# Optimization experiments

Measured on AMD Instinct MI355X. Metric: run time of the kernel, lower is better.

Reference implementation:

```python
import jax, jax.numpy as jnp
import numpy as np

N = 20000   # nodes
E = 40000   # directed edges
F_IN = 13   # dataset.num_features
G = 1000    # graphs in batch
DIMS = [(13, 32), (32, 64), (64, 64)]  # (M_in, M_out) per NNConv layer


def setup_inputs() -> dict:
    key = jax.random.key(0)
    ks = list(jax.random.split(key, 32))
    inp = {}
    inp["x"] = jax.random.normal(ks[0], (N, F_IN), jnp.float32)
    inp["edge_index"] = jax.random.randint(ks[1], (2, E), 0, N, dtype=jnp.int32)
    inp["edge_attr"] = jax.random.uniform(ks[2], (E, 5), dtype=jnp.float32)
    inp["batch"] = jnp.sort(jax.random.randint(ks[3], (N,), 0, G, dtype=jnp.int32))
    i = 4
    for l, (mi, mo) in enumerate(DIMS):
        inp[f"w1_{l}"] = jax.random.normal(ks[i], (5, 128), jnp.float32) / np.sqrt(5.0).astype(np.float32); i += 1
        inp[f"b1_{l}"] = jnp.zeros((128,), jnp.float32)
        inp[f"w2_{l}"] = jax.random.normal(ks[i], (128, mi * mo), jnp.float32) / np.sqrt(128.0).astype(np.float32); i += 1
        inp[f"b2_{l}"] = jnp.zeros((mi * mo,), jnp.float32)
        inp[f"root_{l}"] = jax.random.normal(ks[i], (mi, mo), jnp.float32) / np.sqrt(float(mi)).astype(np.float32); i += 1
        inp[f"bias_{l}"] = jnp.zeros((mo,), jnp.float32)
    inp["fc1_w"] = jax.random.normal(ks[i], (64, 32), jnp.float32) / 8.0; i += 1
    inp["fc1_b"] = jnp.zeros((32,), jnp.float32)
    inp["fc2_w"] = jax.random.normal(ks[i], (32, 16), jnp.float32) / np.sqrt(32.0).astype(np.float32); i += 1
    inp["fc2_b"] = jnp.zeros((16,), jnp.float32)
    inp["fc3_w"] = jax.random.normal(ks[i], (16, 1), jnp.float32) / 4.0; i += 1
    inp["fc3_b"] = jnp.zeros((1,), jnp.float32)
    return inp


def _nnconv(x, src, dst, edge_attr, w1, b1, w2, b2, root, bias, mi, mo):
    # edge MLP: [E,5] -> [E,128] -> [E, mi*mo] per-edge weight matrices
    h = jax.nn.relu(edge_attr @ w1 + b1)
    We = (h @ w2 + b2).reshape(-1, mi, mo)          # [E, mi, mo]
    msg = jnp.einsum('ei,eio->eo', x[src], We)      # gather + per-edge matmul
    agg = jax.ops.segment_sum(msg, dst, num_segments=x.shape[0])  # scatter-add
    return x @ root + agg + bias                    # NNConv root weight + bias


def _forward(x, edge_index, edge_attr, batch, convs, fc1_w, fc1_b, fc2_w, fc2_b, fc3_w, fc3_b):
    src, dst = edge_index[0], edge_index[1]
    for (mi, mo), (w1, b1, w2, b2, root, bias) in zip(DIMS, convs):
        x = jax.nn.elu(_nnconv(x, src, dst, edge_attr, w1, b1, w2, b2, root, bias, mi, mo))
    # scatter_mean pooling over graphs
    sums = jax.ops.segment_sum(x, batch, num_segments=G)
    cnt = jax.ops.segment_sum(jnp.ones((x.shape[0],), x.dtype), batch, num_segments=G)
    xg = sums / jnp.maximum(cnt, 1.0)[:, None]
    xg = jax.nn.elu(xg @ fc1_w + fc1_b)
    xg = jax.nn.elu(xg @ fc2_w + fc2_b)
    return (xg @ fc3_w + fc3_b).reshape(-1)


def reference(x, edge_index, edge_attr, batch,
              w1_0, b1_0, w2_0, b2_0, root_0, bias_0,
              w1_1, b1_1, w2_1, b2_1, root_1, bias_1,
              w1_2, b1_2, w2_2, b2_2, root_2, bias_2,
              fc1_w, fc1_b, fc2_w, fc2_b, fc3_w, fc3_b):
    convs = [(w1_0, b1_0, w2_0, b2_0, root_0, bias_0),
             (w1_1, b1_1, w2_1, b2_1, root_1, bias_1),
             (w1_2, b1_2, w2_2, b2_2, root_2, bias_2)]
    return _forward(x, edge_index, edge_attr, batch, convs,
                    fc1_w, fc1_b, fc2_w, fc2_b, fc3_w, fc3_b)
```

## Files before the change

### kernel.cpp

```cpp
#include <hip/hip_runtime.h>
#include <stdint.h>
#include <math.h>

typedef _Float16 half8_t __attribute__((ext_vector_type(8)));
typedef float floatx4 __attribute__((ext_vector_type(4)));

#define NN 20000
#define NE 40000
#define NG 1000
#define NBLK 313
#define NSPLIT 4

__global__ __launch_bounds__(256) void prep_fused_kernel(
    const float* __restrict__ x, _Float16* __restrict__ e16,
    const float* __restrict__ w2a, const float* __restrict__ b2a, _Float16* __restrict__ oa,
    const float* __restrict__ w2b, const float* __restrict__ b2b, _Float16* __restrict__ ob,
    const float* __restrict__ w2c, const float* __restrict__ b2c, _Float16* __restrict__ oc,
    int* __restrict__ deg)
{
  if (blockIdx.x < 1250) {
    int idx = blockIdx.x * 256 + threadIdx.x;
    int n = idx >> 4, i = idx & 15;
    e16[idx] = (i < 13) ? (_Float16)x[(size_t)n * 13 + i] : (_Float16)0.f;
    return;
  }
  if (blockIdx.x >= 1680) {
    int n = (blockIdx.x - 1680) * 256 + threadIdx.x;
    if (n < NN) deg[n] = 0;
    return;
  }
  const int TOT0 = 68 * 2 * 64, TOT1 = 132 * 4 * 64, TOT2 = 264 * 4 * 64;
  int idx = (blockIdx.x - 1250) * 256 + threadIdx.x;
  const float *w2, *b2; _Float16* op; int mi, mo, mpsh, CT;
  if (idx < TOT0) { w2 = w2a; b2 = b2a; op = oa; mi = 13; mo = 32; mpsh = 4; CT = 2; }
  else if (idx < TOT0 + TOT1) { idx -= TOT0; w2 = w2b; b2 = b2b; op = ob; mi = 32; mo = 64; mpsh = 5; CT = 4; }
  else if (idx < TOT0 + TOT1 + TOT2) { idx -= TOT0 + TOT1; w2 = w2c; b2 = b2c; op = oc; mi = 64; mo = 64; mpsh = 6; CT = 4; }
  else return;
  int l = idx & 63;
  int ct = (idx >> 6) % CT;
  int c = idx / (64 * CT);
  int q = l >> 4;
  int n = ct * 16 + (l & 15);
  int mask = (1 << mpsh) - 1;
  half8_t v;
#pragma unroll
  for (int j = 0; j < 8; ++j) {
    int r = c * 32 + q * 8 + j;
    int k = r >> mpsh, i = r & mask;
    float f = 0.f;
    if (i < mi) {
      if (k < 128) f = w2[(size_t)(k * mi + i) * mo + n];
      else if (k == 128) f = b2[(size_t)i * mo + n];
    }
    v[j] = (_Float16)f;
  }
  *(half8_t*)(op + (size_t)idx * 8) = v;
}

__global__ __launch_bounds__(256) void deg_kernel(const int* __restrict__ dst, int* __restrict__ deg) {
  int e = blockIdx.x * 256 + threadIdx.x;
  if (e < NE) atomicAdd(&deg[dst[e]], 1);
}

__global__ __launch_bounds__(1024) void scan_kernel(
    const int* __restrict__ deg, int* __restrict__ row_ptr, int* __restrict__ cursor)
{
  constexpr int CH = 20;
  __shared__ int wsum[16];
  int t = threadIdx.x;
  int lane = t & 63, w = t >> 6;
  int base = t * CH;
  int local[CH];
#pragma unroll
  for (int i = 0; i < CH; ++i) {
    int n = base + i;
    local[i] = (n < NN) ? deg[n] : 0;
  }
  int s = 0;
#pragma unroll
  for (int i = 0; i < CH; ++i) s += local[i];
  int sc = s;
#pragma unroll
  for (int d = 1; d < 64; d <<= 1) {
    int v = __shfl_up(sc, d, 64);
    if (lane >= d) sc += v;
  }
  if (lane == 63) wsum[w] = sc;
  __syncthreads();
  if (w == 0 && lane < 16) {
    int v = wsum[lane];
    int scc = v;
#pragma unroll
    for (int d = 1; d < 16; d <<= 1) {
      int u = __shfl_up(scc, d, 64);
      if (lane >= d) scc += u;
    }
    wsum[lane] = scc - v;
  }
  __syncthreads();
  int run = wsum[w] + (sc - s);
#pragma unroll
  for (int i = 0; i < CH; ++i) {
    int n = base + i;
    if (n < NN) { row_ptr[n] = run; cursor[n] = run; run += local[i]; }
    else if (n == NN) row_ptr[NN] = run;
  }
}

__global__ __launch_bounds__(256) void fill_kernel(
    const int* __restrict__ dst, int* __restrict__ cursor, int* __restrict__ eids)
{
  int e = blockIdx.x * 256 + threadIdx.x;
  if (e < NE) { int p = atomicAdd(&cursor[dst[e]], 1); eids[p] = e; }
}

template <int MIP, int MO, int NCC, int KCNT>
__global__ __launch_bounds__(256, 4) void msg9_kernel(
    const float* __restrict__ ea, const float* __restrict__ w1,
    const float* __restrict__ b1, const _Float16* __restrict__ xe,
    const int* __restrict__ src,
    const _Float16* __restrict__ w2h, _Float16* __restrict__ msgp)
{
  constexpr int EPB = 128;
  constexpr int CT = MO / 16;
  constexpr int CHB = CT * 1024;
  constexpr int XV = (MIP == 64) ? 2 : 1;
  constexpr int KH = (KCNT + 1) >> 1;

  __shared__ uint4 wsb[2][CHB / 16];
  __shared__ _Float16 h16[KCNT * EPB];
  __shared__ float w1s[5 * 128 + 128];

  const int t = threadIdx.x;
  const int wave = t >> 6, lane = t & 63;
  const int l15 = lane & 15, q = lane >> 4;
  const int split = blockIdx.x / NBLK;
  const int e0 = (blockIdx.x % NBLK) * EPB;
  const int c0 = NCC * split;
  const int kg0 = KCNT * split;

  const char* wgp = (const char*)w2h + (size_t)c0 * CHB;
  uint4 ra4, rb4; uint2 ra2, rb2;
  if constexpr (CT == 4) {
    ra4 = *(const uint4*)(wgp + t * 16);
    rb4 = *(const uint4*)(wgp + CHB + t * 16);
  } else {
    ra2 = *(const uint2*)(wgp + t * 8);
    rb2 = *(const uint2*)(wgp + CHB + t * 8);
  }

  const int wbase = wave * 32;
  half8_t xf[2][XV];
#pragma unroll
  for (int s = 0; s < 2; ++s) {
    int eg = e0 + wbase + s * 16 + l15; if (eg >= NE) eg = NE - 1;
    const _Float16* xr = xe + (size_t)src[eg] * MIP;
    int i0 = (MIP == 16) ? (q & 1) * 8 : q * 8;
    xf[s][0] = *(const half8_t*)(xr + i0);
    if constexpr (MIP == 64)
      xf[s][XV - 1] = *(const half8_t*)(xr + 32 + q * 8);
  }

  const int te = t & 127;
  float ear[5];
  {
    int eg = e0 + te; if (eg >= NE) eg = NE - 1;
#pragma unroll
    for (int j = 0; j < 5; ++j) ear[j] = ea[(size_t)eg * 5 + j];
  }
  for (int i = t; i < 768; i += 256) w1s[i] = (i < 640) ? w1[i] : b1[i - 640];
  __syncthreads();

  {
    int kh = t >> 7;
    int klo = kh * KH;
    int khi = klo + KH; if (khi > KCNT) khi = KCNT;
    for (int kl = klo; kl < khi; ++kl) {
      int kg = kg0 + kl;
      float v;
      if (kg < 128) {
        v = w1s[640 + kg];
#pragma unroll
        for (int j = 0; j < 5; ++j) v = fmaf(ear[j], w1s[j * 128 + kg], v);
        v = fmaxf(v, 0.f);
      } else v = (kg == 128) ? 1.f : 0.f;
      h16[kl * EPB + te] = (_Float16)v;
    }
  }
  __syncthreads();

  floatx4 acc[2][CT];
#pragma unroll
  for (int s = 0; s < 2; ++s)
#pragma unroll
    for (int b = 0; b < CT; ++b) acc[s][b] = (floatx4){0.f, 0.f, 0.f, 0.f};

#pragma unroll 2
  for (int cc = 0; cc < NCC; ++cc) {
    const bool odd = (cc & 1) != 0;
    if constexpr (CT == 4) wsb[cc & 1][t] = odd ? rb4 : ra4;
    else ((uint2*)wsb[cc & 1])[t] = odd ? rb2 : ra2;
    if (cc + 2 < NCC) {
      const char* np = wgp + (size_t)(cc + 2) * CHB;
      if constexpr (CT == 4) {
        if (odd) rb4 = *(const uint4*)(np + t * 16); else ra4 = *(const uint4*)(np + t * 16);
      } else {
        if (odd) rb2 = *(const uint2*)(np + t * 8); else ra2 = *(const uint2*)(np + t * 8);
      }
    }
    __syncthreads();
    const _Float16* wb = (const _Float16*)wsb[cc & 1];
    half8_t bf[CT];
#pragma unroll
    for (int b = 0; b < CT; ++b)
      bf[b] = *(const half8_t*)(wb + (b * 64 + lane) * 8);
    int kl;
    if constexpr (MIP == 64) kl = cc >> 1;
    else if constexpr (MIP == 32) kl = cc;
    else kl = 2 * cc + (q >> 1);
#pragma unroll
    for (int s = 0; s < 2; ++s) {
      _Float16 hv = h16[kl * EPB + wbase + s * 16 + l15];
      half8_t af;
      if constexpr (MIP == 64) af = xf[s][cc & 1] * hv;
      else af = xf[s][0] * hv;
#pragma unroll
      for (int b = 0; b < CT; ++b)
        acc[s][b] = __builtin_amdgcn_mfma_f32_16x16x32_f16(af, bf[b], acc[s][b], 0, 0, 0);
    }
  }

#pragma unroll
  for (int s = 0; s < 2; ++s) {
    int rowb = wbase + s * 16 + q * 4;
#pragma unroll
    for (int b = 0; b < CT; ++b) {
      int n = b * 16 + l15;
#pragma unroll
      for (int r = 0; r < 4; ++r) {
        int row = rowb + r;
        int e = e0 + row;
        if (e < NE) msgp[((size_t)e * NSPLIT + split) * MO + n] = (_Float16)acc[s][b][r];
      }
    }
  }
}

template <int MIP, int NCC, int KCNT>
__global__ __launch_bounds__(256, 4) void msg9p_kernel(
    const float* __restrict__ ea, const float* __restrict__ w1,
    const float* __restrict__ b1, const _Float16* __restrict__ xe,
    const int* __restrict__ src,
    const _Float16* __restrict__ w2h, _Float16* __restrict__ msgp)
{
  constexpr int EPB = 128;
  constexpr int MO = 64;
  constexpr int CT = 4;
  constexpr int CHB = 4096;
  constexpr int XV = (MIP == 64) ? 2 : 1;
  constexpr int KH = (KCNT + 1) >> 1;
  static_assert((NCC & 1) == 0, "NCC must be even for paired chunks");

  __shared__ uint4 wsb[2][2][CHB / 16];
  __shared__ _Float16 h16[KCNT * EPB];
  __shared__ float w1s[5 * 128 + 128];

  const int t = threadIdx.x;
  const int wave = t >> 6, lane = t & 63;
  const int l15 = lane & 15, q = lane >> 4;
  const int split = blockIdx.x / NBLK;
  const int e0 = (blockIdx.x % NBLK) * EPB;
  const int c0 = NCC * split;
  const int kg0 = KCNT * split;

  const char* wgp = (const char*)w2h + (size_t)c0 * CHB;
  uint4 pA0 = *(const uint4*)(wgp + 0 * CHB + t * 16);
  uint4 pA1 = *(const uint4*)(wgp + 1 * CHB + t * 16);
  uint4 pB0 = *(const uint4*)(wgp + 2 * CHB + t * 16);
  uint4 pB1 = *(const uint4*)(wgp + 3 * CHB + t * 16);

  const int wbase = wave * 32;
  half8_t xf[2][XV];
#pragma unroll
  for (int s = 0; s < 2; ++s) {
    int eg = e0 + wbase + s * 16 + l15; if (eg >= NE) eg = NE - 1;
    const _Float16* xr = xe + (size_t)src[eg] * MIP;
    xf[s][0] = *(const half8_t*)(xr + q * 8);
    if constexpr (MIP == 64)
      xf[s][XV - 1] = *(const half8_t*)(xr + 32 + q * 8);
  }

  const int te = t & 127;
  float ear[5];
  {
    int eg = e0 + te; if (eg >= NE) eg = NE - 1;
#pragma unroll
    for (int j = 0; j < 5; ++j) ear[j] = ea[(size_t)eg * 5 + j];
  }
  for (int i = t; i < 768; i += 256) w1s[i] = (i < 640) ? w1[i] : b1[i - 640];
  __syncthreads();

  {
    int kh = t >> 7;
    int klo = kh * KH;
    int khi = klo + KH; if (khi > KCNT) khi = KCNT;
    for (int kl = klo; kl < khi; ++kl) {
      int kg = kg0 + kl;
      float v;
      if (kg < 128) {
        v = w1s[640 + kg];
#pragma unroll
        for (int j = 0; j < 5; ++j) v = fmaf(ear[j], w1s[j * 128 + kg], v);
        v = fmaxf(v, 0.f);
      } else v = (kg == 128) ? 1.f : 0.f;
      h16[kl * EPB + te] = (_Float16)v;
    }
  }
  __syncthreads();

  floatx4 acc[2][CT];
#pragma unroll
  for (int s = 0; s < 2; ++s)
#pragma unroll
    for (int b = 0; b < CT; ++b) acc[s][b] = (floatx4){0.f, 0.f, 0.f, 0.f};

#pragma unroll 2
  for (int ci = 0; ci < NCC / 2; ++ci) {
    const bool odd = (ci & 1) != 0;
    wsb[ci & 1][0][t] = odd ? pB0 : pA0;
    wsb[ci & 1][1][t] = odd ? pB1 : pA1;
    if (2 * ci + 4 < NCC) {
      const char* np = wgp + (size_t)(2 * ci + 4) * CHB;
      if (odd) pB0 = *(const uint4*)(np + t * 16); else pA0 = *(const uint4*)(np + t * 16);
    }
    if (2 * ci + 5 < NCC) {
      const char* np = wgp + (size_t)(2 * ci + 5) * CHB;
      if (odd) pB1 = *(const uint4*)(np + t * 16); else pA1 = *(const uint4*)(np + t * 16);
    }
    __syncthreads();
#pragma unroll
    for (int u = 0; u < 2; ++u) {
      const int cc = 2 * ci + u;
      const _Float16* wbu = (const _Float16*)wsb[ci & 1][u];
      half8_t bf[CT];
#pragma unroll
      for (int b = 0; b < CT; ++b)
        bf[b] = *(const half8_t*)(wbu + (b * 64 + lane) * 8);
      int kl;
      if constexpr (MIP == 64) kl = cc >> 1;
      else kl = cc;
#pragma unroll
      for (int s = 0; s < 2; ++s) {
        _Float16 hv = h16[kl * EPB + wbase + s * 16 + l15];
        half8_t af;
        if constexpr (MIP == 64) af = xf[s][cc & 1] * hv;
        else af = xf[s][0] * hv;
#pragma unroll
        for (int b = 0; b < CT; ++b)
          acc[s][b] = __builtin_amdgcn_mfma_f32_16x16x32_f16(af, bf[b], acc[s][b], 0, 0, 0);
      }
    }
  }

#pragma unroll
  for (int s = 0; s < 2; ++s) {
    int rowb = wbase + s * 16 + q * 4;
#pragma unroll
    for (int b = 0; b < CT; ++b) {
      int n = b * 16 + l15;
#pragma unroll
      for (int r = 0; r < 4; ++r) {
        int row = rowb + r;
        int e = e0 + row;
        if (e < NE) msgp[((size_t)e * NSPLIT + split) * MO + n] = (_Float16)acc[s][b][r];
      }
    }
  }
}

template <int MIN_, int XST, int MO, int FINAL>
__global__ __launch_bounds__(256) void gather_kernel(
    const _Float16* __restrict__ e16in, const float* __restrict__ root,
    const float* __restrict__ bias, const int* __restrict__ row_ptr,
    const int* __restrict__ eids, const _Float16* __restrict__ msgp,
    _Float16* __restrict__ oute, float* __restrict__ outf)
{
  constexpr int NPB = 256 / MO;
  int n = blockIdx.x * NPB + threadIdx.x / MO;
  int o = threadIdx.x % MO;
  if (n >= NN) return;
  float a = bias[o];
#pragma unroll
  for (int i = 0; i < MIN_; ++i)
    a = fmaf((float)e16in[(size_t)n * XST + i], root[i * MO + o], a);
  int r0 = row_ptr[n], r1 = row_ptr[n + 1];
  for (int j = r0; j < r1; ++j) {
    int e = eids[j];
    const _Float16* ep = msgp + (size_t)e * NSPLIT * MO + o;
#pragma unroll
    for (int s = 0; s < NSPLIT; ++s)
      a += (float)ep[s * MO];
  }
  if constexpr (FINAL) {
    outf[(size_t)n * MO + o] = a;
  } else {
    float v = a > 0.f ? a : (expf(a) - 1.f);
    oute[(size_t)n * MO + o] = (_Float16)v;
  }
}

__global__ __launch_bounds__(64) void pool_fc_kernel(
    const float* __restrict__ xn2, const int* __restrict__ batch,
    const float* __restrict__ f1w, const float* __restrict__ f1b,
    const float* __restrict__ f2w, const float* __restrict__ f2b,
    const float* __restrict__ f3w, const float* __restrict__ f3b,
    float* __restrict__ out)
{
  __shared__ float xg[64]; __shared__ float a1[32]; __shared__ float a2[16];
  int g = blockIdx.x, t = threadIdx.x;
  int lo = 0, hi = NN;
  while (lo < hi) { int m = (lo + hi) >> 1; if (batch[m] < g) lo = m + 1; else hi = m; }
  int start = lo; hi = NN;
  while (lo < hi) { int m = (lo + hi) >> 1; if (batch[m] <= g) lo = m + 1; else hi = m; }
  int end = lo;
  float acc = 0.f;
  for (int n = start; n < end; ++n) {
    float v = xn2[(size_t)n * 64 + t];
    acc += v > 0.f ? v : (expf(v) - 1.f);
  }
  float c = (end > start) ? (float)(end - start) : 1.f;
  xg[t] = acc / c;
  __syncthreads();
  if (t < 32) {
    float a = f1b[t];
    for (int i = 0; i < 64; ++i) a = fmaf(xg[i], f1w[i * 32 + t], a);
    a1[t] = a > 0.f ? a : (expf(a) - 1.f);
  }
  __syncthreads();
  if (t < 16) {
    float a = f2b[t];
    for (int i = 0; i < 32; ++i) a = fmaf(a1[i], f2w[i * 16 + t], a);
    a2[t] = a > 0.f ? a : (expf(a) - 1.f);
  }
  __syncthreads();
  if (t == 0) {
    float a = f3b[0];
    for (int i = 0; i < 16; ++i) a = fmaf(a2[i], f3w[i], a);
    out[g] = a;
  }
}

extern "C" void kernel_launch(void* const* d_in, const int* in_sizes, int n_in,
                              void* d_out, int out_size, void* d_ws, size_t ws_size,
                              hipStream_t stream)
{
  const float* x_in  = (const float*)d_in[0];
  const int*   ei    = (const int*)d_in[1];
  const float* ea    = (const float*)d_in[2];
  const int*   batch = (const int*)d_in[3];
  const float* W1[3] = {(const float*)d_in[4],  (const float*)d_in[10], (const float*)d_in[16]};
  const float* B1[3] = {(const float*)d_in[5],  (const float*)d_in[11], (const float*)d_in[17]};
  const float* W2[3] = {(const float*)d_in[6],  (const float*)d_in[12], (const float*)d_in[18]};
  const float* B2[3] = {(const float*)d_in[7],  (const float*)d_in[13], (const float*)d_in[19]};
  const float* RT[3] = {(const float*)d_in[8],  (const float*)d_in[14], (const float*)d_in[20]};
  const float* BS[3] = {(const float*)d_in[9],  (const float*)d_in[15], (const float*)d_in[21]};
  const float* f1w = (const float*)d_in[22]; const float* f1b = (const float*)d_in[23];
  const float* f2w = (const float*)d_in[24]; const float* f2b = (const float*)d_in[25];
  const float* f3w = (const float*)d_in[26]; const float* f3b = (const float*)d_in[27];

  char* ws = (char*)d_ws;
  size_t off = 0;
  auto alloc = [&](size_t bytes) { void* p = ws + off; off += (bytes + 255) & ~(size_t)255; return p; };
  float*    xn2   = (float*)alloc((size_t)NN * 64 * 4);
  _Float16* e16_0 = (_Float16*)alloc((size_t)NN * 16 * 2);
  _Float16* e16_1 = (_Float16*)alloc((size_t)NN * 32 * 2);
  _Float16* e16_2 = (_Float16*)alloc((size_t)NN * 64 * 2);
  _Float16* w2h0  = (_Float16*)alloc((size_t)68 * 2048);
  _Float16* w2h1  = (_Float16*)alloc((size_t)132 * 4096);
  _Float16* w2h2  = (_Float16*)alloc((size_t)264 * 4096);
  _Float16* msgp  = (_Float16*)alloc((size_t)NSPLIT * NE * 64 * 2);
  int*      deg     = (int*)alloc((size_t)NN * 4);
  int*      row_ptr = (int*)alloc((size_t)(NN + 1) * 4);
  int*      cursor  = (int*)alloc((size_t)NN * 4);
  int*      eids    = (int*)alloc((size_t)NE * 4);

  const int* srcp = ei;
  const int* dstp = ei + NE;

  prep_fused_kernel<<<1680 + (NN + 255) / 256, 256, 0, stream>>>(
      x_in, e16_0, W2[0], B2[0], w2h0, W2[1], B2[1], w2h1, W2[2], B2[2], w2h2, deg);
  deg_kernel<<<(NE + 255) / 256, 256, 0, stream>>>(dstp, deg);
  scan_kernel<<<1, 1024, 0, stream>>>(deg, row_ptr, cursor);
  fill_kernel<<<(NE + 255) / 256, 256, 0, stream>>>(dstp, cursor, eids);

  msg9_kernel<16, 32, 17, 34><<<NBLK * NSPLIT, 256, 0, stream>>>(
      ea, W1[0], B1[0], e16_0, srcp, w2h0, msgp);
  gather_kernel<13, 16, 32, 0><<<(NN + 7) / 8, 256, 0, stream>>>(
      e16_0, RT[0], BS[0], row_ptr, eids, msgp, e16_1, xn2);

  msg9_kernel<32, 64, 33, 33><<<NBLK * NSPLIT, 256, 0, stream>>>(
      ea, W1[1], B1[1], e16_1, srcp, w2h1, msgp);
  gather_kernel<32, 32, 64, 0><<<(NN + 3) / 4, 256, 0, stream>>>(
      e16_1, RT[1], BS[1], row_ptr, eids, msgp, e16_2, xn2);

  msg9p_kernel<64, 66, 33><<<NBLK * NSPLIT, 256, 0, stream>>>(
      ea, W1[2], B1[2], e16_2, srcp, w2h2, msgp);
  gather_kernel<64, 64, 64, 1><<<(NN + 3) / 4, 256, 0, stream>>>(
      e16_2, RT[2], BS[2], row_ptr, eids, msgp, e16_2, xn2);

  pool_fc_kernel<<<NG, 64, 0, stream>>>(xn2, batch, f1w, f1b, f2w, f2b, f3w, f3b, (float*)d_out);
}
```

Baseline: 286.2 us.

## Fuse CSR degree count, scan and fill into prep and first message kernels

Degree counting and the prefix scan move into block 0 of the prep kernel, which does the counts with shared-memory atomics instead of global ones. The CSR fill runs as extra blocks appended to the first msg9 launch. This removes three separate kernel launches and their serialization gaps. In exchange, every prep block now reserves about 80KB of LDS, which can limit occupancy, and the single scan block may become the slowest block of the prep launch.

```diff
diff --git a/kernel.cpp b/kernel.cpp
--- a/kernel.cpp
+++ b/kernel.cpp
@@ -11,26 +11,70 @@
 #define NBLK 313
 #define NSPLIT 4
 
-__global__ __launch_bounds__(256) void prep_fused_kernel(
+__global__ __launch_bounds__(1024) void prep_csr_kernel(
     const float* __restrict__ x, _Float16* __restrict__ e16,
     const float* __restrict__ w2a, const float* __restrict__ b2a, _Float16* __restrict__ oa,
     const float* __restrict__ w2b, const float* __restrict__ b2b, _Float16* __restrict__ ob,
     const float* __restrict__ w2c, const float* __restrict__ b2c, _Float16* __restrict__ oc,
-    int* __restrict__ deg)
+    const int* __restrict__ dst, int* __restrict__ row_ptr, int* __restrict__ cursor)
 {
-  if (blockIdx.x < 1250) {
-    int idx = blockIdx.x * 256 + threadIdx.x;
+  __shared__ int sdeg[20480];
+  __shared__ int wsum[16];
+
+  if (blockIdx.x == 0) {
+    constexpr int CH = 20;
+    int t = threadIdx.x;
+    int lane = t & 63, w = t >> 6;
+    for (int i = t; i < 20480; i += 1024) sdeg[i] = 0;
+    __syncthreads();
+    for (int e = t; e < NE; e += 1024) atomicAdd(&sdeg[dst[e]], 1);
+    __syncthreads();
+    int base = t * CH;
+    int local[CH];
+#pragma unroll
+    for (int i = 0; i < CH; ++i) local[i] = sdeg[base + i];
+    int s = 0;
+#pragma unroll
+    for (int i = 0; i < CH; ++i) s += local[i];
+    int sc = s;
+#pragma unroll
+    for (int d = 1; d < 64; d <<= 1) {
+      int v = __shfl_up(sc, d, 64);
+      if (lane >= d) sc += v;
+    }
+    if (lane == 63) wsum[w] = sc;
+    __syncthreads();
+    if (w == 0 && lane < 16) {
+      int v = wsum[lane];
+      int scc = v;
+#pragma unroll
+      for (int d = 1; d < 16; d <<= 1) {
+        int u = __shfl_up(scc, d, 64);
+        if (lane >= d) scc += u;
+      }
+      wsum[lane] = scc - v;
+    }
+    __syncthreads();
+    int run = wsum[w] + (sc - s);
+#pragma unroll
+    for (int i = 0; i < CH; ++i) {
+      int n = base + i;
+      if (n < NN) { row_ptr[n] = run; cursor[n] = run; run += local[i]; }
+      else if (n == NN) row_ptr[NN] = run;
+    }
+    return;
+  }
+
+  if (blockIdx.x <= 313) {
+    int idx = (blockIdx.x - 1) * 1024 + threadIdx.x;
+    if (idx >= NN * 16) return;
     int n = idx >> 4, i = idx & 15;
     e16[idx] = (i < 13) ? (_Float16)x[(size_t)n * 13 + i] : (_Float16)0.f;
     return;
   }
-  if (blockIdx.x >= 1680) {
-    int n = (blockIdx.x - 1680) * 256 + threadIdx.x;
-    if (n < NN) deg[n] = 0;
-    return;
-  }
+
   const int TOT0 = 68 * 2 * 64, TOT1 = 132 * 4 * 64, TOT2 = 264 * 4 * 64;
-  int idx = (blockIdx.x - 1250) * 256 + threadIdx.x;
+  int idx = (blockIdx.x - 314) * 1024 + threadIdx.x;
   const float *w2, *b2; _Float16* op; int mi, mo, mpsh, CT;
   if (idx < TOT0) { w2 = w2a; b2 = b2a; op = oa; mi = 13; mo = 32; mpsh = 4; CT = 2; }
   else if (idx < TOT0 + TOT1) { idx -= TOT0; w2 = w2b; b2 = b2b; op = ob; mi = 32; mo = 64; mpsh = 5; CT = 4; }
@@ -57,70 +101,21 @@
   *(half8_t*)(op + (size_t)idx * 8) = v;
 }
 
-__global__ __launch_bounds__(256) void deg_kernel(const int* __restrict__ dst, int* __restrict__ deg) {
-  int e = blockIdx.x * 256 + threadIdx.x;
-  if (e < NE) atomicAdd(&deg[dst[e]], 1);
-}
-
-__global__ __launch_bounds__(1024) void scan_kernel(
-    const int* __restrict__ deg, int* __restrict__ row_ptr, int* __restrict__ cursor)
-{
-  constexpr int CH = 20;
-  __shared__ int wsum[16];
-  int t = threadIdx.x;
-  int lane = t & 63, w = t >> 6;
-  int base = t * CH;
-  int local[CH];
-#pragma unroll
-  for (int i = 0; i < CH; ++i) {
-    int n = base + i;
-    local[i] = (n < NN) ? deg[n] : 0;
-  }
-  int s = 0;
-#pragma unroll
-  for (int i = 0; i < CH; ++i) s += local[i];
-  int sc = s;
-#pragma unroll
-  for (int d = 1; d < 64; d <<= 1) {
-    int v = __shfl_up(sc, d, 64);
-    if (lane >= d) sc += v;
-  }
-  if (lane == 63) wsum[w] = sc;
-  __syncthreads();
-  if (w == 0 && lane < 16) {
-    int v = wsum[lane];
-    int scc = v;
-#pragma unroll
-    for (int d = 1; d < 16; d <<= 1) {
-      int u = __shfl_up(scc, d, 64);
-      if (lane >= d) scc += u;
-    }
-    wsum[lane] = scc - v;
-  }
-  __syncthreads();
-  int run = wsum[w] + (sc - s);
-#pragma unroll
-  for (int i = 0; i < CH; ++i) {
-    int n = base + i;
-    if (n < NN) { row_ptr[n] = run; cursor[n] = run; run += local[i]; }
-    else if (n == NN) row_ptr[NN] = run;
-  }
-}
-
-__global__ __launch_bounds__(256) void fill_kernel(
-    const int* __restrict__ dst, int* __restrict__ cursor, int* __restrict__ eids)
-{
-  int e = blockIdx.x * 256 + threadIdx.x;
-  if (e < NE) { int p = atomicAdd(&cursor[dst[e]], 1); eids[p] = e; }
-}
-
-template <int MIP, int MO, int NCC, int KCNT>
+template <int MIP, int MO, int NCC, int KCNT, int FILLB>
 __global__ __launch_bounds__(256, 4) void msg9_kernel(
     const float* __restrict__ ea, const float* __restrict__ w1,
     const float* __restrict__ b1, const _Float16* __restrict__ xe,
     const int* __restrict__ src,
-    const _Float16* __restrict__ w2h, _Float16* __restrict__ msgp)
+    const _Float16* __restrict__ w2h, _Float16* __restrict__ msgp,
+    const int* __restrict__ dst, int* __restrict__ cursor, int* __restrict__ eids)
 {
+  if constexpr (FILLB) {
+    if (blockIdx.x >= NBLK * NSPLIT) {
+      int e = (blockIdx.x - NBLK * NSPLIT) * 256 + threadIdx.x;
+      if (e < NE) { int p = atomicAdd(&cursor[dst[e]], 1); eids[p] = e; }
+      return;
+    }
+  }
   constexpr int EPB = 128;
   constexpr int CT = MO / 16;
   constexpr int CHB = CT * 1024;
@@ -479,7 +474,6 @@
   _Float16* w2h1  = (_Float16*)alloc((size_t)132 * 4096);
   _Float16* w2h2  = (_Float16*)alloc((size_t)264 * 4096);
   _Float16* msgp  = (_Float16*)alloc((size_t)NSPLIT * NE * 64 * 2);
-  int*      deg     = (int*)alloc((size_t)NN * 4);
   int*      row_ptr = (int*)alloc((size_t)(NN + 1) * 4);
   int*      cursor  = (int*)alloc((size_t)NN * 4);
   int*      eids    = (int*)alloc((size_t)NE * 4);
@@ -487,19 +481,17 @@
   const int* srcp = ei;
   const int* dstp = ei + NE;
 
-  prep_fused_kernel<<<1680 + (NN + 255) / 256, 256, 0, stream>>>(
-      x_in, e16_0, W2[0], B2[0], w2h0, W2[1], B2[1], w2h1, W2[2], B2[2], w2h2, deg);
-  deg_kernel<<<(NE + 255) / 256, 256, 0, stream>>>(dstp, deg);
-  scan_kernel<<<1, 1024, 0, stream>>>(deg, row_ptr, cursor);
-  fill_kernel<<<(NE + 255) / 256, 256, 0, stream>>>(dstp, cursor, eids);
-
-  msg9_kernel<16, 32, 17, 34><<<NBLK * NSPLIT, 256, 0, stream>>>(
-      ea, W1[0], B1[0], e16_0, srcp, w2h0, msgp);
+  prep_csr_kernel<<<422, 1024, 0, stream>>>(
+      x_in, e16_0, W2[0], B2[0], w2h0, W2[1], B2[1], w2h1, W2[2], B2[2], w2h2,
+      dstp, row_ptr, cursor);
+
+  msg9_kernel<16, 32, 17, 34, 1><<<NBLK * NSPLIT + 157, 256, 0, stream>>>(
+      ea, W1[0], B1[0], e16_0, srcp, w2h0, msgp, dstp, cursor, eids);
   gather_kernel<13, 16, 32, 0><<<(NN + 7) / 8, 256, 0, stream>>>(
       e16_0, RT[0], BS[0], row_ptr, eids, msgp, e16_1, xn2);
 
-  msg9_kernel<32, 64, 33, 33><<<NBLK * NSPLIT, 256, 0, stream>>>(
-      ea, W1[1], B1[1], e16_1, srcp, w2h1, msgp);
+  msg9_kernel<32, 64, 33, 33, 0><<<NBLK * NSPLIT, 256, 0, stream>>>(
+      ea, W1[1], B1[1], e16_1, srcp, w2h1, msgp, nullptr, nullptr, nullptr);
   gather_kernel<32, 32, 64, 0><<<(NN + 3) / 4, 256, 0, stream>>>(
       e16_1, RT[1], BS[1], row_ptr, eids, msgp, e16_2, xn2);
 
```

After: 282.4 us. No clear change (-1.3%).
